# Performance work log

Hardware: AMD Instinct MI355X
Metric: run time of the kernel (lower is better)

Reference implementation:

```python
import jax, jax.numpy as jnp
import numpy as np

N, E, B = 131072, 262144, 4096
NODE_DIM, EDGE_DIM, HIDDEN = 16, 4, 64
MLP_HID = 128


def setup_inputs() -> dict:
    key = jax.random.key(0)
    ks = jax.random.split(key, 16)
    def nrm(k, shape, s=0.05):
        return jax.random.normal(k, shape, jnp.float32) * s
    return {
        "x": jax.random.normal(ks[0], (N, NODE_DIM), jnp.float32),
        "edge_attr": jax.random.normal(ks[1], (E, EDGE_DIM), jnp.float32),
        "edge_index": jax.random.randint(ks[2], (2, E), 0, N),
        "batch": jnp.sort(jax.random.randint(ks[3], (N,), 0, B)),
        "w_e1": nrm(ks[4], (EDGE_DIM, MLP_HID)),
        "b_e1": jnp.zeros((MLP_HID,), jnp.float32),
        "w_e2": nrm(ks[5], (MLP_HID, NODE_DIM * HIDDEN)),
        "b_e2": jnp.zeros((NODE_DIM * HIDDEN,), jnp.float32),
        "root": nrm(ks[6], (NODE_DIM, HIDDEN)),
        "conv_bias": jnp.zeros((HIDDEN,), jnp.float32),
        "gru_wih": nrm(ks[7], (3 * HIDDEN, HIDDEN)),
        "gru_whh": nrm(ks[8], (3 * HIDDEN, HIDDEN)),
        "gru_bih": jnp.zeros((3 * HIDDEN,), jnp.float32),
        "gru_bhh": jnp.zeros((3 * HIDDEN,), jnp.float32),
        "lstm_wih": nrm(ks[9], (4 * HIDDEN, 2 * HIDDEN)),
        "lstm_whh": nrm(ks[10], (4 * HIDDEN, HIDDEN)),
        "lstm_bih": jnp.zeros((4 * HIDDEN,), jnp.float32),
        "lstm_bhh": jnp.zeros((4 * HIDDEN,), jnp.float32),
        "fc1_w": nrm(ks[11], (2 * HIDDEN, HIDDEN)),
        "fc1_b": jnp.zeros((HIDDEN,), jnp.float32),
        "fc2_w": nrm(ks[12], (HIDDEN, 1)),
        "fc2_b": jnp.zeros((1,), jnp.float32),
    }


def reference(x, edge_attr, edge_index, batch,
              w_e1, b_e1, w_e2, b_e2, root, conv_bias,
              gru_wih, gru_whh, gru_bih, gru_bhh,
              lstm_wih, lstm_whh, lstm_bih, lstm_bhh,
              fc1_w, fc1_b, fc2_w, fc2_b):
    src, dst = edge_index[0], edge_index[1]
    # NNConv: edge-MLP -> per-edge weight [E, node_dim, hidden]
    Wdyn = (jax.nn.relu(edge_attr @ w_e1 + b_e1) @ w_e2 + b_e2).reshape(E, NODE_DIM, HIDDEN)
    msg = jnp.einsum('ed,edh->eh', x[src], Wdyn)  # gather + per-edge matmul
    msum = jax.ops.segment_sum(msg, dst, num_segments=N)
    cnt = jax.ops.segment_sum(jnp.ones((E,), msg.dtype), dst, num_segments=N)
    agg = msum / jnp.maximum(cnt, 1.0)[:, None]  # scatter-mean
    out = jax.nn.relu(agg + x @ root + conv_bias)
    h = out
    for _ in range(3):
        gi = out @ gru_wih.T + gru_bih
        gh = h @ gru_whh.T + gru_bhh
        ir, iz, inn = jnp.split(gi, 3, axis=-1)
        hr, hz, hn = jnp.split(gh, 3, axis=-1)
        r = jax.nn.sigmoid(ir + hr)
        z = jax.nn.sigmoid(iz + hz)
        n = jnp.tanh(inn + r * hn)
        h = (1.0 - z) * n + z * h
        out = h
    # Set2Set, 3 processing steps
    hl = jnp.zeros((B, HIDDEN), out.dtype)
    cl = jnp.zeros((B, HIDDEN), out.dtype)
    q_star = jnp.zeros((B, 2 * HIDDEN), out.dtype)
    for _ in range(3):
        gates = q_star @ lstm_wih.T + lstm_bih + hl @ lstm_whh.T + lstm_bhh
        ig, fg, gg, og = jnp.split(gates, 4, axis=-1)
        ig = jax.nn.sigmoid(ig); fg = jax.nn.sigmoid(fg)
        gg = jnp.tanh(gg); og = jax.nn.sigmoid(og)
        cl = fg * cl + ig * gg
        hl = og * jnp.tanh(cl)
        q = hl  # [B, H]
        e = jnp.sum(out * q[batch], axis=-1)  # [N]
        m = jax.lax.stop_gradient(jax.ops.segment_max(e, batch, num_segments=B))
        ex = jnp.exp(e - m[batch])
        denom = jax.ops.segment_sum(ex, batch, num_segments=B)
        a = ex / denom[batch]  # segment softmax
        r_g = jax.ops.segment_sum(a[:, None] * out, batch, num_segments=B)
        q_star = jnp.concatenate([q, r_g], axis=-1)
    y = jax.nn.relu(q_star @ fc1_w + fc1_b)
    return (y @ fc2_w + fc2_b).squeeze(-1)
```

## Files before the change

### kernel.cpp

```cpp
#include <hip/hip_runtime.h>
#include <math.h>

#define N_NODES 131072
#define N_EDGES 262144
#define N_B     4096

typedef __attribute__((ext_vector_type(8))) short short8;
typedef __attribute__((ext_vector_type(8))) _Float16 half8;
typedef __attribute__((ext_vector_type(4))) float f32x4;
typedef __attribute__((ext_vector_type(16))) float f32x16;

__device__ __forceinline__ float fast_sig(float x) {
    return 1.0f / (1.0f + __expf(-x));
}
__device__ __forceinline__ float fast_tanh(float x) {
    float t = __expf(-2.0f * fabsf(x));
    float r = (1.0f - t) / (1.0f + t);
    return copysignf(r, x);
}

__device__ __forceinline__ void load_lds16(const void* g, void* l) {
    __builtin_amdgcn_global_load_lds(
        (const __attribute__((address_space(1))) unsigned int*)g,
        (__attribute__((address_space(3))) unsigned int*)l, 16, 0, 0);
}

__global__ __launch_bounds__(256) void k_misc(
    const float* __restrict__ we2, unsigned short* __restrict__ wt,
    const float* __restrict__ gwih, const float* __restrict__ gwhh,
    const float* __restrict__ gbih, const float* __restrict__ gbhh,
    unsigned short* __restrict__ wtg, float* __restrict__ gbias,
    const float* __restrict__ lwih, const float* __restrict__ lwhh,
    float4* __restrict__ wA, float4* __restrict__ wB,
    const int* __restrict__ batch, int* __restrict__ starts,
    const int* __restrict__ eidx, int* __restrict__ deg)
{
    const int bid = blockIdx.x;
    const int tid = threadIdx.x;
    if (bid >= 105) {
        int p = (bid - 105) * 256 + tid;
        atomicAdd(&deg[eidx[N_EDGES + p]], 1);
        return;
    }
    if (bid < 64) {
        int p = bid * 256 + tid;
        int d = p >> 10;
        int u = (p >> 9) & 1;
        int s = (p >> 6) & 7;
        int l = p & 63;
        int k0 = s * 16 + ((l >> 5) << 3);
        int h = u * 32 + (l & 31);
        half8 hv;
        #pragma unroll
        for (int j = 0; j < 8; ++j) {
            float v = we2[(size_t)(k0 + j) * 1024 + d * 64 + h];
            hv[j] = (_Float16)v;
        }
        size_t base = (size_t)d * 8192 + (size_t)u * 4096 + s * 512 + l * 8;
        *(half8*)&wt[base] = hv;
    } else if (bid < 72) {
        int p = (bid - 64) * 256 + tid;
        if (p < 256) {
            int g = p >> 6, j = p & 63;
            float b;
            if (g == 0)      b = gbih[j] + gbhh[j];
            else if (g == 1) b = gbih[64 + j] + gbhh[64 + j];
            else if (g == 2) b = gbih[128 + j];
            else             b = gbhh[128 + j];
            gbias[p] = b;
        }
        int u = p >> 7, ks = (p >> 6) & 1, ln = p & 63;
        int n = u * 16 + (ln & 15);
        int g = n >> 6, jn = n & 63;
        int k0 = ks * 32 + (ln >> 4) * 8;
        half8 hv;
        #pragma unroll
        for (int jj = 0; jj < 8; ++jj) {
            int k = k0 + jj;
            float v;
            if (g == 0)      v = gwih[jn * 64 + k] + gwhh[jn * 64 + k];
            else if (g == 1) v = gwih[(64 + jn) * 64 + k] + gwhh[(64 + jn) * 64 + k];
            else if (g == 2) v = gwih[(128 + jn) * 64 + k];
            else             v = gwhh[(128 + jn) * 64 + k];
            hv[jj] = (_Float16)v;
        }
        size_t base = (size_t)(u * 2 + ks) * 512 + ln * 8;
        *(half8*)&wtg[base] = hv;
    } else if (bid < 88) {
        int p = (bid - 72) * 256 + tid;
        int k = p >> 6, ln = p & 63;
        float4 a, b;
        a.x = lwih[(0 * 64 + ln) * 128 + k] + lwhh[(0 * 64 + ln) * 64 + k];
        a.y = lwih[(1 * 64 + ln) * 128 + k] + lwhh[(1 * 64 + ln) * 64 + k];
        a.z = lwih[(2 * 64 + ln) * 128 + k] + lwhh[(2 * 64 + ln) * 64 + k];
        a.w = lwih[(3 * 64 + ln) * 128 + k] + lwhh[(3 * 64 + ln) * 64 + k];
        b.x = lwih[(0 * 64 + ln) * 128 + 64 + k];
        b.y = lwih[(1 * 64 + ln) * 128 + 64 + k];
        b.z = lwih[(2 * 64 + ln) * 128 + 64 + k];
        b.w = lwih[(3 * 64 + ln) * 128 + 64 + k];
        wA[p] = a; wB[p] = b;
    } else {
        int g = (bid - 88) * 256 + tid;
        if (g > N_B) return;
        if (g == N_B) { starts[N_B] = N_NODES; return; }
        int lo = 0, hi = N_NODES;
        while (lo < hi) {
            int mid = (lo + hi) >> 1;
            if (batch[mid] < g) lo = mid + 1; else hi = mid;
        }
        starts[g] = lo;
    }
}

__global__ __launch_bounds__(256) void k_scan1(
    const int* __restrict__ deg, int* __restrict__ psum)
{
    __shared__ int sm[256];
    const int t = threadIdx.x;
    sm[t] = deg[blockIdx.x * 256 + t];
    __syncthreads();
    #pragma unroll
    for (int off = 128; off; off >>= 1) {
        if (t < off) sm[t] += sm[t + off];
        __syncthreads();
    }
    if (t == 0) psum[blockIdx.x] = sm[0];
}

__global__ __launch_bounds__(512) void k_scan2(
    const int* __restrict__ psum, int* __restrict__ psumx)
{
    __shared__ int sm[512];
    const int t = threadIdx.x;
    sm[t] = psum[t];
    __syncthreads();
    #pragma unroll
    for (int off = 1; off < 512; off <<= 1) {
        int add = (t >= off) ? sm[t - off] : 0;
        __syncthreads();
        sm[t] += add;
        __syncthreads();
    }
    psumx[t] = (t > 0) ? sm[t - 1] : 0;
}

__global__ __launch_bounds__(256) void k_scan3(
    const int* __restrict__ deg, const int* __restrict__ psumx,
    int* __restrict__ row_ptr, int* __restrict__ cursor)
{
    __shared__ int sm[256];
    const int t = threadIdx.x;
    const int i = blockIdx.x * 256 + t;
    int d = deg[i];
    sm[t] = d;
    __syncthreads();
    #pragma unroll
    for (int off = 1; off < 256; off <<= 1) {
        int add = (t >= off) ? sm[t - off] : 0;
        __syncthreads();
        sm[t] += add;
        __syncthreads();
    }
    int excl = sm[t] - d + psumx[blockIdx.x];
    row_ptr[i] = excl;
    cursor[i] = excl;
    if (i == 0) row_ptr[N_NODES] = N_EDGES;
}

__global__ __launch_bounds__(256) void k_scat(
    const int* __restrict__ eidx, int* __restrict__ cursor,
    int* __restrict__ epos)
{
    int e = blockIdx.x * 256 + threadIdx.x;
    int dst = eidx[N_EDGES + e];
    epos[e] = atomicAdd(&cursor[dst], 1);
}

__global__ __launch_bounds__(512)
__attribute__((amdgpu_waves_per_eu(4, 8)))
void k_edge(
    const float* __restrict__ x,
    const float* __restrict__ ea,
    const int*   __restrict__ eidx,
    const int*   __restrict__ epos,
    const float* __restrict__ we1,
    const float* __restrict__ be1,
    const unsigned short* __restrict__ wt,
    const float* __restrict__ be2,
    float* __restrict__ emsg)
{
    __shared__ unsigned short sAh[16384];
    __shared__ unsigned short sB[2][8192];
    __shared__ float sxT[16 * 136];
    __shared__ float sbe2[1024];
    __shared__ int   spos[128];

    const int tid = threadIdx.x;
    const int w   = tid >> 6;
    const int ln  = tid & 63;
    const int u   = w >> 2;
    const int mt  = w & 3;
    const int eb  = blockIdx.x * 128;
    const int d0  = blockIdx.x & 15;

    #pragma unroll
    for (int r = 0; r < 2; ++r) {
        int seg = r * 8 + w;
        load_lds16(wt + (size_t)d0 * 8192 + seg * 512 + ln * 8,
                   &sB[0][seg * 512]);
    }

    if (tid < 128) spos[tid] = epos[eb + tid];
    #pragma unroll
    for (int v = tid; v < 1024; v += 512) sbe2[v] = be2[v];

    {
        int e = tid >> 2, q = tid & 3;
        int src = eidx[eb + e];
        float4 t4 = ((const float4*)(x + (size_t)src * 16))[q];
        sxT[(q * 4 + 0) * 136 + e] = t4.x;
        sxT[(q * 4 + 1) * 136 + e] = t4.y;
        sxT[(q * 4 + 2) * 136 + e] = t4.z;
        sxT[(q * 4 + 3) * 136 + e] = t4.w;
    }

    #pragma unroll 1
    for (int i = 0; i < 4; ++i) {
        int cc = tid + i * 512;
        int mtc = cc >> 9;
        int s  = (cc >> 6) & 7;
        int l  = cc & 63;
        int e   = mtc * 32 + (l & 31);
        int kk0 = s * 16 + ((l >> 5) << 3);
        float4 eav = *(const float4*)(ea + (size_t)(eb + e) * 4);
        float4 b0 = *(const float4*)(be1 + kk0);
        float4 b1 = *(const float4*)(be1 + kk0 + 4);
        float acc[8] = {b0.x, b0.y, b0.z, b0.w, b1.x, b1.y, b1.z, b1.w};
        #pragma unroll
        for (int a = 0; a < 4; ++a) {
            float4 wa0 = *(const float4*)(we1 + a * 128 + kk0);
            float4 wa1 = *(const float4*)(we1 + a * 128 + kk0 + 4);
            float ev = (a == 0) ? eav.x : (a == 1) ? eav.y : (a == 2) ? eav.z : eav.w;
            acc[0] += ev * wa0.x; acc[1] += ev * wa0.y;
            acc[2] += ev * wa0.z; acc[3] += ev * wa0.w;
            acc[4] += ev * wa1.x; acc[5] += ev * wa1.y;
            acc[6] += ev * wa1.z; acc[7] += ev * wa1.w;
        }
        half8 hv;
        #pragma unroll
        for (int j = 0; j < 8; ++j) {
            hv[j] = (_Float16)fmaxf(acc[j], 0.0f);
        }
        *(half8*)&sAh[cc * 8] = hv;
    }
    __syncthreads();

    half8 ah[8];
    #pragma unroll
    for (int s = 0; s < 8; ++s) {
        ah[s] = *(half8*)&sAh[((mt * 8 + s) * 64 + ln) * 8];
    }
    #pragma unroll
    for (int s = 0; s < 8; ++s) {
        asm volatile("" : "+v"(ah[s]));
    }

    const int rbase = (ln >> 5) * 4;

    f32x16 msg;
    #pragma unroll
    for (int r = 0; r < 16; ++r) msg[r] = 0.0f;

    #pragma unroll 1
    for (int dd = 0; dd < 16; ++dd) {
        const int d = (d0 + dd) & 15;
        const int cur = dd & 1;

        if (dd < 15) {
            int dn = (d + 1) & 15;
            #pragma unroll
            for (int r = 0; r < 2; ++r) {
                int seg = r * 8 + w;
                load_lds16(wt + (size_t)dn * 8192 + seg * 512 + ln * 8,
                           &sB[cur ^ 1][seg * 512]);
            }
        }

        float bv = sbe2[d * 64 + u * 32 + (ln & 31)];
        f32x16 c2;
        #pragma unroll
        for (int r = 0; r < 16; ++r) c2[r] = bv;

        #pragma unroll
        for (int s = 0; s < 8; ++s) {
            half8 bb = *(half8*)&sB[cur][u * 4096 + s * 512 + ln * 8];
            c2 = __builtin_amdgcn_mfma_f32_32x32x16_f16(ah[s], bb, c2, 0, 0, 0);
        }
        #pragma unroll
        for (int q = 0; q < 4; ++q) {
            f32x4 xv = *(const f32x4*)&sxT[d * 136 + mt * 32 + rbase + 8 * q];
            #pragma unroll
            for (int j = 0; j < 4; ++j) {
                msg[q * 4 + j] = fmaf(xv[j], c2[q * 4 + j], msg[q * 4 + j]);
            }
        }
        __syncthreads();
    }

    const int col = u * 32 + (ln & 31);
    #pragma unroll
    for (int r = 0; r < 16; ++r) {
        int row = (r & 3) + ((r >> 2) * 8) + rbase;
        int pos = spos[mt * 32 + row];
        emsg[(size_t)pos * 64 + col] = msg[r];
    }
}

__global__ __launch_bounds__(256, 2) void k_gru2(
    float* __restrict__ buf,
    const float* __restrict__ emsg,
    const int* __restrict__ rowp,
    const float* __restrict__ x,
    const float* __restrict__ root,
    const float* __restrict__ cb,
    const unsigned short* __restrict__ wtg,
    const float* __restrict__ gbias)
{
    __shared__ unsigned short sAh[8192];
    __shared__ float sroot[1024];
    __shared__ float sbias[256];
    __shared__ float scb[64];
    const int tid = threadIdx.x;
    const int w = tid >> 6, ln = tid & 63, lq = ln >> 4, lm = ln & 15;
    const size_t nbase = (size_t)blockIdx.x * 128;

    #pragma unroll
    for (int v = tid; v < 1024; v += 256) sroot[v] = root[v];
    sbias[tid] = gbias[tid];
    if (tid < 64) scb[tid] = cb[tid];
    __syncthreads();

    #pragma unroll 2
    for (int i = 0; i < 4; ++i) {
        int cc = tid + i * 256;
        int mt = cc >> 7, ks = (cc >> 6) & 1, l = cc & 63;
        size_t gn = nbase + mt * 16 + (l & 15);
        int c0 = ks * 32 + (l >> 4) * 8;
        int rp0 = rowp[gn], rp1 = rowp[gn + 1];
        float ms[8] = {0.f, 0.f, 0.f, 0.f, 0.f, 0.f, 0.f, 0.f};
        for (int k = rp0; k < rp1; ++k) {
            float4 m0 = *(const float4*)(emsg + (size_t)k * 64 + c0);
            float4 m1 = *(const float4*)(emsg + (size_t)k * 64 + c0 + 4);
            ms[0] += m0.x; ms[1] += m0.y; ms[2] += m0.z; ms[3] += m0.w;
            ms[4] += m1.x; ms[5] += m1.y; ms[6] += m1.z; ms[7] += m1.w;
        }
        float cinv = 1.0f / fmaxf((float)(rp1 - rp0), 1.0f);
        float xv[16];
        *(float4*)&xv[0]  = *(const float4*)(x + gn * 16);
        *(float4*)&xv[4]  = *(const float4*)(x + gn * 16 + 4);
        *(float4*)&xv[8]  = *(const float4*)(x + gn * 16 + 8);
        *(float4*)&xv[12] = *(const float4*)(x + gn * 16 + 12);
        float acc[8];
        #pragma unroll
        for (int j = 0; j < 8; ++j) acc[j] = scb[c0 + j];
        #pragma unroll
        for (int d = 0; d < 16; ++d) {
            float xd = xv[d];
            #pragma unroll
            for (int j = 0; j < 8; ++j) acc[j] += xd * sroot[d * 64 + c0 + j];
        }
        half8 hv;
        #pragma unroll
        for (int j = 0; j < 8; ++j) {
            float hval = fmaxf(ms[j] * cinv + acc[j], 0.0f);
            hv[j] = (_Float16)hval;
        }
        *(half8*)&sAh[cc * 8] = hv;
    }
    __syncthreads();

    #pragma unroll 1
    for (int step = 0; step < 3; ++step) {
        half8 ah[2][2];
        #pragma unroll
        for (int i = 0; i < 2; ++i)
            #pragma unroll
            for (int ks = 0; ks < 2; ++ks) {
                int mt = w * 2 + i;
                ah[i][ks] = *(half8*)&sAh[((mt * 2 + ks) * 64 + ln) * 8];
            }
        __syncthreads();

        #pragma unroll 1
        for (int v = 0; v < 4; ++v) {
            f32x4 C[4][2];
            #pragma unroll
            for (int g = 0; g < 4; ++g) {
                float bv = sbias[g * 64 + v * 16 + lm];
                #pragma unroll
                for (int i = 0; i < 2; ++i) C[g][i] = (f32x4){bv, bv, bv, bv};
            }
            #pragma unroll
            for (int g = 0; g < 4; ++g) {
                int u = g * 4 + v;
                #pragma unroll
                for (int ks = 0; ks < 2; ++ks) {
                    size_t wb = (size_t)(u * 2 + ks) * 512 + ln * 8;
                    half8 bb = *(const half8*)&wtg[wb];
                    #pragma unroll
                    for (int i = 0; i < 2; ++i) {
                        C[g][i] = __builtin_amdgcn_mfma_f32_16x16x32_f16(ah[i][ks], bb, C[g][i], 0, 0, 0);
                    }
                }
            }
            int ksp = v >> 1;
            int lq2 = (v & 1) * 2 + (lm >> 3);
            int jp = lm & 7;
            #pragma unroll
            for (int i = 0; i < 2; ++i) {
                int mt = w * 2 + i;
                #pragma unroll
                for (int r = 0; r < 4; ++r) {
                    int idx = ((mt * 2 + ksp) * 64 + lq2 * 16 + lq * 4 + r) * 8 + jp;
                    float hold = (float)*(const _Float16*)&sAh[idx];
                    float rr = fast_sig(C[0][i][r]);
                    float zz = fast_sig(C[1][i][r]);
                    float nn = fast_tanh(C[2][i][r] + rr * C[3][i][r]);
                    float hnew = (1.0f - zz) * nn + zz * hold;
                    if (step < 2) {
                        _Float16 hh = (_Float16)hnew;
                        sAh[idx] = *(unsigned short*)&hh;
                    } else {
                        buf[(nbase + mt * 16 + lq * 4 + r) * 64 + v * 16 + lm] = hnew;
                    }
                }
            }
        }
        if (step < 2) __syncthreads();
    }
}

__global__ __launch_bounds__(256) void k_s2s(
    const float* __restrict__ out,
    const int*   __restrict__ starts,
    const float4* __restrict__ wA,
    const float4* __restrict__ wB,
    const float* __restrict__ bih,
    const float* __restrict__ bhh,
    const float* __restrict__ fc1w,
    const float* __restrict__ fc1b,
    const float* __restrict__ fc2w,
    const float* __restrict__ fc2b,
    float* __restrict__ y)
{
    __shared__ float osh[4][32][66];
    __shared__ float qsL[4][128];
    __shared__ float ebuf[4][256];
    const int tid = threadIdx.x;
    const int wv = tid >> 6, ln = tid & 63;
    const int gid = blockIdx.x * 4 + wv;

    const int s0 = starts[gid];
    int L = starts[gid + 1] - s0; if (L > 256) L = 256;
    const int SL = (L < 32) ? L : 32;

    #pragma unroll
    for (int base = 0; base < 32; base += 4) {
        int row = base + (ln >> 4);
        int c4 = (ln & 15) * 4;
        if (row < SL)
            *(float4*)&osh[wv][row][c4] =
                *(const float4*)(out + (size_t)(s0 + row) * 64 + c4);
    }

    qsL[wv][ln] = 0.0f; qsL[wv][64 + ln] = 0.0f;
    __builtin_amdgcn_wave_barrier();

    const float b0 = bih[ln] + bhh[ln];
    const float b1 = bih[64 + ln] + bhh[64 + ln];
    const float b2 = bih[128 + ln] + bhh[128 + ln];
    const float b3 = bih[192 + ln] + bhh[192 + ln];

    float c = 0.0f;

    #pragma unroll 1
    for (int step = 0; step < 3; ++step) {
        float a0 = b0, a1 = b1, a2 = b2, a3 = b3;
        #pragma unroll 4
        for (int k = 0; k < 64; ++k) {
            float qk = qsL[wv][k];
            float rk = qsL[wv][64 + k];
            float4 wa = wA[k * 64 + ln];
            float4 wb = wB[k * 64 + ln];
            a0 += wa.x * qk + wb.x * rk;
            a1 += wa.y * qk + wb.y * rk;
            a2 += wa.z * qk + wb.z * rk;
            a3 += wa.w * qk + wb.w * rk;
        }
        float ig = fast_sig(a0), fg = fast_sig(a1);
        float gg = fast_tanh(a2), og = fast_sig(a3);
        c = fg * c + ig * gg;
        float h = og * fast_tanh(c);
        __builtin_amdgcn_wave_barrier();
        qsL[wv][ln] = h;
        __builtin_amdgcn_wave_barrier();

        float m = -1e30f;
        for (int c0 = 0; c0 * 64 < L; ++c0) {
            int j = c0 * 64 + ln;
            if (j < L) {
                float a = 0.0f;
                if (j < SL) {
                    #pragma unroll
                    for (int l4 = 0; l4 < 16; ++l4) {
                        float4 ov = *(const float4*)&osh[wv][j][l4 * 4];
                        float4 hv = *(const float4*)&qsL[wv][l4 * 4];
                        a += ov.x * hv.x + ov.y * hv.y + ov.z * hv.z + ov.w * hv.w;
                    }
                } else {
                    const float4* orow = (const float4*)(out + (size_t)(s0 + j) * 64);
                    #pragma unroll
                    for (int l4 = 0; l4 < 16; ++l4) {
                        float4 ov = orow[l4];
                        float4 hv = *(const float4*)&qsL[wv][l4 * 4];
                        a += ov.x * hv.x + ov.y * hv.y + ov.z * hv.z + ov.w * hv.w;
                    }
                }
                ebuf[wv][j] = a;
                m = fmaxf(m, a);
            }
        }
        #pragma unroll
        for (int off = 32; off; off >>= 1) m = fmaxf(m, __shfl_xor(m, off));
        float ds = 0.0f;
        for (int c0 = 0; c0 * 64 < L; ++c0) {
            int j = c0 * 64 + ln;
            if (j < L) {
                float ex = __expf(ebuf[wv][j] - m);
                ebuf[wv][j] = ex;
                ds += ex;
            }
        }
        #pragma unroll
        for (int off = 32; off; off >>= 1) ds += __shfl_xor(ds, off);
        __builtin_amdgcn_wave_barrier();
        float rg = 0.0f;
        for (int j = 0; j < SL; ++j)
            rg = fmaf(ebuf[wv][j], osh[wv][j][ln], rg);
        for (int j = SL; j < L; ++j)
            rg = fmaf(ebuf[wv][j], out[(size_t)(s0 + j) * 64 + ln], rg);
        rg = (L > 0) ? (rg / ds) : 0.0f;
        qsL[wv][64 + ln] = rg;
        __builtin_amdgcn_wave_barrier();
    }

    float a = fc1b[ln];
    #pragma unroll 4
    for (int k = 0; k < 128; ++k)
        a = fmaf(qsL[wv][k], fc1w[k * 64 + ln], a);
    float uu = fmaxf(a, 0.0f) * fc2w[ln];
    #pragma unroll
    for (int off = 32; off; off >>= 1) uu += __shfl_xor(uu, off);
    if (ln == 0) y[gid] = uu + fc2b[0];
}

extern "C" void kernel_launch(void* const* d_in, const int* in_sizes, int n_in,
                              void* d_out, int out_size, void* d_ws, size_t ws_size,
                              hipStream_t stream) {
    const float* x     = (const float*)d_in[0];
    const float* ea    = (const float*)d_in[1];
    const int*   eidx  = (const int*)d_in[2];
    const int*   batch = (const int*)d_in[3];
    const float* we1   = (const float*)d_in[4];
    const float* be1   = (const float*)d_in[5];
    const float* we2   = (const float*)d_in[6];
    const float* be2   = (const float*)d_in[7];
    const float* root  = (const float*)d_in[8];
    const float* cb    = (const float*)d_in[9];
    const float* gwih  = (const float*)d_in[10];
    const float* gwhh  = (const float*)d_in[11];
    const float* gbih  = (const float*)d_in[12];
    const float* gbhh  = (const float*)d_in[13];
    const float* lwih  = (const float*)d_in[14];
    const float* lwhh  = (const float*)d_in[15];
    const float* lbih  = (const float*)d_in[16];
    const float* lbhh  = (const float*)d_in[17];
    const float* fc1w  = (const float*)d_in[18];
    const float* fc1b  = (const float*)d_in[19];
    const float* fc2w  = (const float*)d_in[20];
    const float* fc2b  = (const float*)d_in[21];

    float* emsg = (float*)d_ws;
    float* buf  = emsg + (size_t)N_EDGES * 64;
    int* deg    = (int*)(buf + (size_t)N_NODES * 64);
    int* cursor = deg + N_NODES;
    int* rowp   = cursor + N_NODES;
    int* epos   = rowp + N_NODES + 1;
    int* psum   = epos + N_EDGES;
    int* psumx  = psum + 512;
    int* starts = psumx + 512;
    size_t off = (size_t)((char*)(starts + N_B + 1) - (char*)d_ws);
    off = (off + 15) & ~(size_t)15;
    unsigned short* wt  = (unsigned short*)((char*)d_ws + off);
    unsigned short* wtg = wt + 262144;
    float* gbias = (float*)(wtg + 32768);
    float4* wA = (float4*)(gbias + 256);
    float4* wB = wA + 4096;
    float* y = (float*)d_out;

    hipMemsetAsync(deg, 0, (size_t)N_NODES * sizeof(int), stream);
    k_misc<<<1129, 256, 0, stream>>>(we2, wt, gwih, gwhh, gbih, gbhh, wtg, gbias,
                                     lwih, lwhh, wA, wB, batch, starts, eidx, deg);
    k_scan1<<<512, 256, 0, stream>>>(deg, psum);
    k_scan2<<<1, 512, 0, stream>>>(psum, psumx);
    k_scan3<<<512, 256, 0, stream>>>(deg, psumx, rowp, cursor);
    k_scat<<<1024, 256, 0, stream>>>(eidx, cursor, epos);
    k_edge<<<N_EDGES / 128, 512, 0, stream>>>(x, ea, eidx, epos, we1, be1, wt, be2, emsg);
    k_gru2<<<N_NODES / 128, 256, 0, stream>>>(buf, emsg, rowp, x, root, cb,
                                              wtg, gbias);
    k_s2s<<<N_B / 4, 256, 0, stream>>>(buf, starts, wA, wB, lbih, lbhh,
                                       fc1w, fc1b, fc2w, fc2b, y);
}
```

Measured before the change: 354.2 us.

## Triple-buffer edge weight tiles in LDS, reusing sAh region after A-load

Replaces the double-buffered B-tile pipeline in the edge kernel with a triple buffer. The third buffer reuses the sAh LDS region once its fragments are in registers. Prefetch now runs two steps ahead with explicit vmcnt waits and a single raw barrier per iteration instead of a trailing __syncthreads. The aim is to hide global-to-LDS latency behind MFMA work, at the cost of hand-managed waitcnt correctness and an extra barrier before the loop.

```diff
diff --git a/kernel.cpp b/kernel.cpp
--- a/kernel.cpp
+++ b/kernel.cpp
@@ -189,11 +189,11 @@
     const float* __restrict__ be2,
     float* __restrict__ emsg)
 {
-    __shared__ unsigned short sAh[16384];
-    __shared__ unsigned short sB[2][8192];
-    __shared__ float sxT[16 * 136];
-    __shared__ float sbe2[1024];
-    __shared__ int   spos[128];
+    __shared__ __attribute__((aligned(16))) char smem[62464];
+    unsigned short* sAh  = (unsigned short*)smem;
+    float* sxT  = (float*)(smem + 49152);
+    float* sbe2 = (float*)(smem + 57856);
+    int*   spos = (int*)(smem + 61952);
 
     const int tid = threadIdx.x;
     const int w   = tid >> 6;
@@ -207,7 +207,7 @@
     for (int r = 0; r < 2; ++r) {
         int seg = r * 8 + w;
         load_lds16(wt + (size_t)d0 * 8192 + seg * 512 + ln * 8,
-                   &sB[0][seg * 512]);
+                   smem + 32768 + seg * 1024);
     }
 
     if (tid < 128) spos[tid] = epos[eb + tid];
@@ -264,6 +264,17 @@
     for (int s = 0; s < 8; ++s) {
         asm volatile("" : "+v"(ah[s]));
     }
+    __syncthreads();
+
+    {
+        int dn = (d0 + 1) & 15;
+        #pragma unroll
+        for (int r = 0; r < 2; ++r) {
+            int seg = r * 8 + w;
+            load_lds16(wt + (size_t)dn * 8192 + seg * 512 + ln * 8,
+                       smem + 0 + seg * 1024);
+        }
+    }
 
     const int rbase = (ln >> 5) * 4;
 
@@ -271,20 +282,18 @@
     #pragma unroll
     for (int r = 0; r < 16; ++r) msg[r] = 0.0f;
 
+    int m = 0;
     #pragma unroll 1
     for (int dd = 0; dd < 16; ++dd) {
         const int d = (d0 + dd) & 15;
-        const int cur = dd & 1;
-
-        if (dd < 15) {
-            int dn = (d + 1) & 15;
-            #pragma unroll
-            for (int r = 0; r < 2; ++r) {
-                int seg = r * 8 + w;
-                load_lds16(wt + (size_t)dn * 8192 + seg * 512 + ln * 8,
-                           &sB[cur ^ 1][seg * 512]);
-            }
-        }
+
+        if (dd == 15) asm volatile("s_waitcnt vmcnt(0)" ::: "memory");
+        else          asm volatile("s_waitcnt vmcnt(2)" ::: "memory");
+        __builtin_amdgcn_s_barrier();
+        __builtin_amdgcn_sched_barrier(0);
+
+        const unsigned short* bcur =
+            (const unsigned short*)(smem + (m == 0 ? 32768 : (m == 1 ? 0 : 16384)));
 
         float bv = sbe2[d * 64 + u * 32 + (ln & 31)];
         f32x16 c2;
@@ -293,7 +302,7 @@
 
         #pragma unroll
         for (int s = 0; s < 8; ++s) {
-            half8 bb = *(half8*)&sB[cur][u * 4096 + s * 512 + ln * 8];
+            half8 bb = *(const half8*)&bcur[u * 4096 + s * 512 + ln * 8];
             c2 = __builtin_amdgcn_mfma_f32_32x32x16_f16(ah[s], bb, c2, 0, 0, 0);
         }
         #pragma unroll
@@ -304,7 +313,19 @@
                 msg[q * 4 + j] = fmaf(xv[j], c2[q * 4 + j], msg[q * 4 + j]);
             }
         }
-        __syncthreads();
+
+        if (dd + 2 < 16) {
+            int dn = (d0 + dd + 2) & 15;
+            int mn = (m == 0) ? 2 : (m == 1 ? 0 : 1);
+            char* db = smem + (mn == 0 ? 32768 : (mn == 1 ? 0 : 16384));
+            #pragma unroll
+            for (int r = 0; r < 2; ++r) {
+                int seg = r * 8 + w;
+                load_lds16(wt + (size_t)dn * 8192 + seg * 512 + ln * 8,
+                           db + seg * 1024);
+            }
+        }
+        m = (m == 2) ? 0 : m + 1;
     }
 
     const int col = u * 32 + (ln & 31);
```

Measured after the change: 354.3 us. About the same (+0.0%).
